# Optimization experiments

Measured on AMD Instinct MI355X. Metric: run time of the kernel, lower is better.

Reference implementation:

```python
import jax, jax.numpy as jnp
import numpy as np

DIM = 2048
SEQ = 8192
NUM_HEADS = 16
PROJ_DIM = DIM // 4  # proj_ratio = 4.0
EPS = 1e-5


def setup_inputs() -> dict:
    key = jax.random.key(0)
    ks = jax.random.split(key, 8)
    s = 0.02  # param init scale
    return {
        "x": jax.random.normal(ks[0], (SEQ, DIM), jnp.float32),
        "q": jax.random.normal(ks[1], (1, DIM), jnp.float32),
        "W_kv": jax.random.normal(ks[2], (2 * DIM, DIM), jnp.float32) * s,
        "b_kv": jax.random.normal(ks[3], (2 * DIM,), jnp.float32) * s,
        "W_p1": jax.random.normal(ks[4], (PROJ_DIM, DIM), jnp.float32) * s,
        "b_p1": jax.random.normal(ks[5], (PROJ_DIM,), jnp.float32) * s,
        "W_p2": jax.random.normal(ks[6], (DIM, PROJ_DIM), jnp.float32) * s,
        "b_p2": jax.random.normal(ks[7], (DIM,), jnp.float32) * s,
        "ln_w": jnp.ones((PROJ_DIM,), jnp.float32),
        "ln_b": jnp.zeros((PROJ_DIM,), jnp.float32),
    }


def reference(x, q, W_kv, b_kv, W_p1, b_p1, W_p2, b_p2, ln_w, ln_b):
    seq, dim = x.shape
    h = NUM_HEADS
    d = dim // h

    # kv projection: [s, 2*dim]; split '(n h d)' with n leading -> k = first dim cols
    kv = x @ W_kv.T + b_kv
    k = kv[:, :dim].reshape(seq, h, d).transpose(1, 0, 2)   # [h, s, d]
    v = kv[:, dim:].reshape(seq, h, d).transpose(1, 0, 2)   # [h, s, d]
    qh = q.reshape(h, 1, d)                                  # '1 (h d) -> h 1 d'

    # single-query attention (qk_norm=False -> Identity norms)
    attn = jnp.einsum('hqd,hkd->hqk', qh, k) / jnp.sqrt(jnp.asarray(d, x.dtype))
    attn = jax.nn.softmax(attn, axis=-1)                     # [h, 1, s]
    x1 = jnp.einsum('hqk,hkd->hqd', attn, v)                 # [h, 1, d]
    x1 = x1.transpose(1, 0, 2).reshape(1, dim)               # 'h s d -> s (h d)'

    # proj MLP: proj1 -> LayerNorm -> relu -> proj2
    h1 = x1 @ W_p1.T + b_p1                                  # [1, proj_dim]
    mu = jnp.mean(h1, axis=-1, keepdims=True)
    var = jnp.mean(jnp.square(h1 - mu), axis=-1, keepdims=True)
    h1 = (h1 - mu) / jnp.sqrt(var + EPS) * ln_w + ln_b
    x1 = jax.nn.relu(h1) @ W_p2.T + b_p2                     # [1, dim]

    # residual broadcast: [s, dim] + [1, dim]
    return x + x1
```

## Files before the change

### kernel.cpp

```cpp
#include <hip/hip_runtime.h>
#include <math.h>

#define SEQ   8192
#define DIM   2048
#define NH    16
#define DH    128
#define PD    512

static constexpr float LN_EPS = 1e-5f;
static constexpr float SCALE  = 0.08838834764831845f;

typedef __bf16 bf16x8 __attribute__((ext_vector_type(8)));
typedef float  f32x4  __attribute__((ext_vector_type(4)));

static constexpr size_t OFF_QB   = 0;
static constexpr size_t OFF_SMP  = 16;
static constexpr size_t OFF_QWB  = 528;
static constexpr size_t OFF_ELOG = 16912;
static constexpr size_t OFF_PCTX = OFF_ELOG + 131072;
static constexpr size_t OFF_CTX  = OFF_PCTX + 2097152;
static constexpr size_t OFF_X1   = OFF_CTX + 32768;
static constexpr size_t OFF_H1R  = OFF_X1 + 2048;
static constexpr size_t OFF_X1F  = OFF_H1R + 512;

__global__ __launch_bounds__(256) void k_prep(const float* __restrict__ q,
                                              const float* __restrict__ Wkv,
                                              const float* __restrict__ bkv,
                                              __bf16* __restrict__ qWb,
                                              float* __restrict__ qb,
                                              float* __restrict__ smp) {
    int t = threadIdx.x;
    int h = blockIdx.x >> 4, jc = blockIdx.x & 15;
    int col = t & 127, kh = t >> 7;
    int j = jc * 128 + col;
    const float* w  = Wkv + (size_t)(h * DH + kh * 64) * DIM + j;
    const float* qh = q + h * DH + kh * 64;
    float acc = 0.f;
#pragma unroll 16
    for (int d = 0; d < 64; ++d)
        acc += qh[d] * __builtin_nontemporal_load(w + (size_t)d * DIM);
    __shared__ float part[128];
    if (kh) part[col] = acc;
    __syncthreads();
    if (!kh) qWb[h * DIM + j] = (__bf16)(acc + part[col]);
    if (jc == 0 && t < 64) {
        float p = q[h*DH + t] * bkv[h*DH + t] + q[h*DH + 64 + t] * bkv[h*DH + 64 + t];
        for (int off = 32; off; off >>= 1) p += __shfl_down(p, off);
        if (t == 0) qb[h] = p;
    }
    if (blockIdx.x == 0) { smp[t] = 0.f; smp[t + 256] = 0.f; }
}

__global__ __launch_bounds__(256) void k_logits(const float* __restrict__ x,
                                                const __bf16* __restrict__ qWb,
                                                const float* __restrict__ qb,
                                                float* __restrict__ elogT,
                                                float* __restrict__ smp) {
    const int t = threadIdx.x;
    const int w = t >> 6, lane = t & 63;
    const int r = lane & 15, quad = lane >> 4;
    const int s0 = blockIdx.x * 16;
    __shared__ float dpart[4][64][4];
    __shared__ float hsum[NH];
    if (t < NH) hsum[t] = 0.f;

    const float*  xrow = x + (size_t)(s0 + r) * DIM + quad * 8;
    const __bf16* brow = qWb + r * DIM + quad * 8;
    const int kbase = w * 512;

    f32x4 acc = {0.f, 0.f, 0.f, 0.f};
#pragma unroll 4
    for (int i = 0; i < 16; ++i) {
        int k = kbase + i * 32;
        float4 xa = *(const float4*)(xrow + k);
        float4 xb = *(const float4*)(xrow + k + 4);
        bf16x8 af;
        af[0] = (__bf16)xa.x; af[1] = (__bf16)xa.y;
        af[2] = (__bf16)xa.z; af[3] = (__bf16)xa.w;
        af[4] = (__bf16)xb.x; af[5] = (__bf16)xb.y;
        af[6] = (__bf16)xb.z; af[7] = (__bf16)xb.w;
        bf16x8 bf = *(const bf16x8*)(brow + k);
        acc = __builtin_amdgcn_mfma_f32_16x16x32_bf16(af, bf, acc, 0, 0, 0);
    }
    dpart[w][lane][0] = acc[0];
    dpart[w][lane][1] = acc[1];
    dpart[w][lane][2] = acc[2];
    dpart[w][lane][3] = acc[3];
    __syncthreads();

    {
        const int lane2 = t & 63, reg = t >> 6;
        const int h = lane2 & 15, sl = (lane2 >> 4) * 4 + reg;
        float v = dpart[0][lane2][reg] + dpart[1][lane2][reg]
                + dpart[2][lane2][reg] + dpart[3][lane2][reg];
        float e = __expf((v + qb[h]) * SCALE);
        elogT[(size_t)(s0 + sl) * NH + h] = e;
        atomicAdd(&hsum[h], e);
    }
    __syncthreads();
    if (t < NH) atomicAdd(&smp[t * 32 + (blockIdx.x & 31)], hsum[t]);
}

__global__ __launch_bounds__(256) void k_wctx(const float* __restrict__ x,
                                              const float* __restrict__ elogT,
                                              float* __restrict__ pctx) {
    const int b = blockIdx.x, t = threadIdx.x;
    const int sc = b >> 3, jc = b & 7;
    const int s0 = sc * 128;
    const int j = jc * 256 + t;

    __shared__ float att[128 * NH];
    for (int i = t; i < 128 * NH; i += 256)
        att[i] = elogT[(size_t)s0 * NH + i];
    __syncthreads();

    float acc[NH];
#pragma unroll
    for (int h = 0; h < NH; ++h) acc[h] = 0.f;
    const float* xp = x + (size_t)s0 * DIM + j;
#pragma unroll 4
    for (int rr = 0; rr < 128; ++rr) {
        float xv = xp[(size_t)rr * DIM];
        const f32x4* ar = (const f32x4*)(att + rr * NH);
        f32x4 a0 = ar[0], a1 = ar[1], a2 = ar[2], a3 = ar[3];
        float aa[NH];
        *(f32x4*)&aa[0] = a0; *(f32x4*)&aa[4]  = a1;
        *(f32x4*)&aa[8] = a2; *(f32x4*)&aa[12] = a3;
#pragma unroll
        for (int h = 0; h < NH; ++h) acc[h] += xv * aa[h];
    }
#pragma unroll
    for (int h = 0; h < NH; ++h)
        __builtin_nontemporal_store(acc[h],
            &pctx[((size_t)(sc * NH + h)) * DIM + j]);
}

__global__ __launch_bounds__(256) void k_ctxred(const float* __restrict__ pctx,
                                                const float* __restrict__ smp,
                                                float* __restrict__ ctx) {
    const int b = blockIdx.x, t = threadIdx.x;
    const int h = b >> 5;
    const int col = t & 63, ch = t >> 6;
    __shared__ float sInv;
    __shared__ float psum[4][64];
    const size_t idx = (size_t)b * 64 + col;
    float s = 0.f;
#pragma unroll
    for (int i = 0; i < 16; ++i)
        s += __builtin_nontemporal_load(
                 &pctx[(size_t)(ch * 16 + i) * (NH * DIM) + idx]);
    psum[ch][col] = s;
    if (t < 32) {
        float v = smp[h * 32 + t];
        for (int off = 16; off; off >>= 1) v += __shfl_xor(v, off);
        if (t == 0) sInv = 1.0f / v;
    }
    __syncthreads();
    if (ch == 0)
        ctx[idx] = (psum[0][col] + psum[1][col] + psum[2][col] + psum[3][col]) * sInv;
}

__global__ __launch_bounds__(256) void k_x1(const float* __restrict__ Wkv,
                                            const float* __restrict__ bkv,
                                            const float* __restrict__ ctx,
                                            float* __restrict__ x1) {
    int row = blockIdx.x * 4 + (threadIdx.x >> 6);
    int lane = threadIdx.x & 63;
    const float* w = Wkv + (size_t)(DIM + row) * DIM;
    const float* c = ctx + (row >> 7) * DIM;
    float acc = 0.f;
#pragma unroll
    for (int k = 0; k < 8; ++k) {
        int j = k * 256 + lane * 4;
        f32x4 wv = __builtin_nontemporal_load((const f32x4*)&w[j]);
        f32x4 cv = *(const f32x4*)&c[j];
        acc += wv[0]*cv[0] + wv[1]*cv[1] + wv[2]*cv[2] + wv[3]*cv[3];
    }
    for (int off = 32; off; off >>= 1) acc += __shfl_xor(acc, off);
    if (lane == 0) x1[row] = acc + bkv[DIM + row];
}

__global__ __launch_bounds__(256) void k_h1(const float* __restrict__ Wp1,
                                            const float* __restrict__ bp1,
                                            const float* __restrict__ x1,
                                            float* __restrict__ h1raw) {
    int row = blockIdx.x * 4 + (threadIdx.x >> 6);
    int lane = threadIdx.x & 63;
    const float* w = Wp1 + (size_t)row * DIM;
    float acc = 0.f;
#pragma unroll
    for (int k = 0; k < 8; ++k) {
        int j = k * 256 + lane * 4;
        f32x4 wv = __builtin_nontemporal_load((const f32x4*)&w[j]);
        f32x4 cv = *(const f32x4*)&x1[j];
        acc += wv[0]*cv[0] + wv[1]*cv[1] + wv[2]*cv[2] + wv[3]*cv[3];
    }
    for (int off = 32; off; off >>= 1) acc += __shfl_xor(acc, off);
    if (lane == 0) h1raw[row] = acc + bp1[row];
}

__global__ __launch_bounds__(256) void k_x1f(const float* __restrict__ Wp2,
                                             const float* __restrict__ bp2,
                                             const float* __restrict__ h1raw,
                                             const float* __restrict__ lnw,
                                             const float* __restrict__ lnb,
                                             float* __restrict__ x1f) {
    int row = blockIdx.x * 4 + (threadIdx.x >> 6);
    int lane = threadIdx.x & 63;
    int j = lane * 8;
    float4 va = *(const float4*)&h1raw[j];
    float4 vb = *(const float4*)&h1raw[j + 4];
    float s = va.x + va.y + va.z + va.w + vb.x + vb.y + vb.z + vb.w;
    for (int off = 32; off; off >>= 1) s += __shfl_xor(s, off);
    float mu = s * (1.0f / PD);
    float dx[8];
    dx[0]=va.x-mu; dx[1]=va.y-mu; dx[2]=va.z-mu; dx[3]=va.w-mu;
    dx[4]=vb.x-mu; dx[5]=vb.y-mu; dx[6]=vb.z-mu; dx[7]=vb.w-mu;
    float s2 = 0.f;
#pragma unroll
    for (int i = 0; i < 8; ++i) s2 += dx[i] * dx[i];
    for (int off = 32; off; off >>= 1) s2 += __shfl_xor(s2, off);
    float rstd = rsqrtf(s2 * (1.0f / PD) + LN_EPS);
    float4 lw0 = *(const float4*)&lnw[j], lw1 = *(const float4*)&lnw[j + 4];
    float4 lb0 = *(const float4*)&lnb[j], lb1 = *(const float4*)&lnb[j + 4];
    float hln[8];
    hln[0]=fmaxf(dx[0]*rstd*lw0.x+lb0.x,0.f); hln[1]=fmaxf(dx[1]*rstd*lw0.y+lb0.y,0.f);
    hln[2]=fmaxf(dx[2]*rstd*lw0.z+lb0.z,0.f); hln[3]=fmaxf(dx[3]*rstd*lw0.w+lb0.w,0.f);
    hln[4]=fmaxf(dx[4]*rstd*lw1.x+lb1.x,0.f); hln[5]=fmaxf(dx[5]*rstd*lw1.y+lb1.y,0.f);
    hln[6]=fmaxf(dx[6]*rstd*lw1.z+lb1.z,0.f); hln[7]=fmaxf(dx[7]*rstd*lw1.w+lb1.w,0.f);
    const float* w = Wp2 + (size_t)row * PD + j;
    f32x4 w0 = __builtin_nontemporal_load((const f32x4*)w);
    f32x4 w1 = __builtin_nontemporal_load((const f32x4*)(w + 4));
    float acc = w0[0]*hln[0] + w0[1]*hln[1] + w0[2]*hln[2] + w0[3]*hln[3]
              + w1[0]*hln[4] + w1[1]*hln[5] + w1[2]*hln[6] + w1[3]*hln[7];
    for (int off = 32; off; off >>= 1) acc += __shfl_xor(acc, off);
    if (lane == 0) x1f[row] = acc + bp2[row];
}

__global__ __launch_bounds__(256) void k_out(const float* __restrict__ x,
                                             const float* __restrict__ x1f,
                                             float* __restrict__ out) {
    size_t i = (size_t)blockIdx.x * 512 + threadIdx.x;
    f32x4 xv = ((const f32x4*)x)[i];
    f32x4 a  = ((const f32x4*)x1f)[(int)(i & 511)];
    __builtin_nontemporal_store(xv + a, (f32x4*)out + i);
    size_t i2 = i + 256;
    f32x4 xv2 = ((const f32x4*)x)[i2];
    f32x4 a2  = ((const f32x4*)x1f)[(int)(i2 & 511)];
    __builtin_nontemporal_store(xv2 + a2, (f32x4*)out + i2);
}

extern "C" void kernel_launch(void* const* d_in, const int* in_sizes, int n_in,
                              void* d_out, int out_size, void* d_ws, size_t ws_size,
                              hipStream_t stream) {
    const float* x    = (const float*)d_in[0];
    const float* q    = (const float*)d_in[1];
    const float* Wkv  = (const float*)d_in[2];
    const float* bkv  = (const float*)d_in[3];
    const float* Wp1  = (const float*)d_in[4];
    const float* bp1  = (const float*)d_in[5];
    const float* Wp2  = (const float*)d_in[6];
    const float* bp2  = (const float*)d_in[7];
    const float* lnw  = (const float*)d_in[8];
    const float* lnb  = (const float*)d_in[9];
    float* out = (float*)d_out;
    float* ws  = (float*)d_ws;

    float*  qb    = ws + OFF_QB;
    float*  smp   = ws + OFF_SMP;
    __bf16* qWb   = (__bf16*)(ws + OFF_QWB);
    float*  elogT = ws + OFF_ELOG;
    float*  pctx  = ws + OFF_PCTX;
    float*  ctx   = ws + OFF_CTX;
    float*  x1    = ws + OFF_X1;
    float*  h1raw = ws + OFF_H1R;
    float*  x1f   = ws + OFF_X1F;

    k_prep  <<<256, 256, 0, stream>>>(q, Wkv, bkv, qWb, qb, smp);
    k_logits<<<512, 256, 0, stream>>>(x, qWb, qb, elogT, smp);
    k_wctx  <<<512, 256, 0, stream>>>(x, elogT, pctx);
    k_ctxred<<<512, 256, 0, stream>>>(pctx, smp, ctx);
    k_x1    <<<512, 256, 0, stream>>>(Wkv, bkv, ctx, x1);
    k_h1    <<<128, 256, 0, stream>>>(Wp1, bp1, x1, h1raw);
    k_x1f   <<<512, 256, 0, stream>>>(Wp2, bp2, h1raw, lnw, lnb, x1f);
    k_out   <<<8192, 256, 0, stream>>>(x, x1f, out);
}
```

Baseline: 214.2 us.

## Replace bf16 MFMA logits kernel with fp32 VALU register-resident qW dot products

After: 249.1 us. +16.3%, slower.

```diff
diff --git a/kernel.cpp b/kernel.cpp
--- a/kernel.cpp
+++ b/kernel.cpp
@@ -10,13 +10,12 @@
 static constexpr float LN_EPS = 1e-5f;
 static constexpr float SCALE  = 0.08838834764831845f;
 
-typedef __bf16 bf16x8 __attribute__((ext_vector_type(8)));
-typedef float  f32x4  __attribute__((ext_vector_type(4)));
+typedef float f32x4 __attribute__((ext_vector_type(4)));
 
 static constexpr size_t OFF_QB   = 0;
 static constexpr size_t OFF_SMP  = 16;
-static constexpr size_t OFF_QWB  = 528;
-static constexpr size_t OFF_ELOG = 16912;
+static constexpr size_t OFF_QWT  = 528;
+static constexpr size_t OFF_ELOG = OFF_QWT + 32768;
 static constexpr size_t OFF_PCTX = OFF_ELOG + 131072;
 static constexpr size_t OFF_CTX  = OFF_PCTX + 2097152;
 static constexpr size_t OFF_X1   = OFF_CTX + 32768;
@@ -26,7 +25,7 @@
 __global__ __launch_bounds__(256) void k_prep(const float* __restrict__ q,
                                               const float* __restrict__ Wkv,
                                               const float* __restrict__ bkv,
-                                              __bf16* __restrict__ qWb,
+                                              float* __restrict__ qWT,
                                               float* __restrict__ qb,
                                               float* __restrict__ smp) {
     int t = threadIdx.x;
@@ -42,7 +41,7 @@
     __shared__ float part[128];
     if (kh) part[col] = acc;
     __syncthreads();
-    if (!kh) qWb[h * DIM + j] = (__bf16)(acc + part[col]);
+    if (!kh) qWT[(size_t)j * NH + h] = acc + part[col];
     if (jc == 0 && t < 64) {
         float p = q[h*DH + t] * bkv[h*DH + t] + q[h*DH + 64 + t] * bkv[h*DH + 64 + t];
         for (int off = 32; off; off >>= 1) p += __shfl_down(p, off);
@@ -51,54 +50,65 @@
     if (blockIdx.x == 0) { smp[t] = 0.f; smp[t + 256] = 0.f; }
 }
 
-__global__ __launch_bounds__(256) void k_logits(const float* __restrict__ x,
-                                                const __bf16* __restrict__ qWb,
-                                                const float* __restrict__ qb,
-                                                float* __restrict__ elogT,
-                                                float* __restrict__ smp) {
-    const int t = threadIdx.x;
+__global__ __launch_bounds__(256) void k_logv(const float* __restrict__ x,
+                                              const float* __restrict__ qWT,
+                                              const float* __restrict__ qb,
+                                              float* __restrict__ elogT,
+                                              float* __restrict__ smp) {
+    const int b = blockIdx.x, t = threadIdx.x;
     const int w = t >> 6, lane = t & 63;
-    const int r = lane & 15, quad = lane >> 4;
-    const int s0 = blockIdx.x * 16;
-    __shared__ float dpart[4][64][4];
+    const int s0 = b * 8;
+
+    __shared__ float wsum[8][4][NH];
     __shared__ float hsum[NH];
     if (t < NH) hsum[t] = 0.f;
 
-    const float*  xrow = x + (size_t)(s0 + r) * DIM + quad * 8;
-    const __bf16* brow = qWb + r * DIM + quad * 8;
-    const int kbase = w * 512;
-
-    f32x4 acc = {0.f, 0.f, 0.f, 0.f};
-#pragma unroll 4
-    for (int i = 0; i < 16; ++i) {
-        int k = kbase + i * 32;
-        float4 xa = *(const float4*)(xrow + k);
-        float4 xb = *(const float4*)(xrow + k + 4);
-        bf16x8 af;
-        af[0] = (__bf16)xa.x; af[1] = (__bf16)xa.y;
-        af[2] = (__bf16)xa.z; af[3] = (__bf16)xa.w;
-        af[4] = (__bf16)xb.x; af[5] = (__bf16)xb.y;
-        af[6] = (__bf16)xb.z; af[7] = (__bf16)xb.w;
-        bf16x8 bf = *(const bf16x8*)(brow + k);
-        acc = __builtin_amdgcn_mfma_f32_16x16x32_bf16(af, bf, acc, 0, 0, 0);
-    }
-    dpart[w][lane][0] = acc[0];
-    dpart[w][lane][1] = acc[1];
-    dpart[w][lane][2] = acc[2];
-    dpart[w][lane][3] = acc[3];
-    __syncthreads();
-
-    {
-        const int lane2 = t & 63, reg = t >> 6;
-        const int h = lane2 & 15, sl = (lane2 >> 4) * 4 + reg;
-        float v = dpart[0][lane2][reg] + dpart[1][lane2][reg]
-                + dpart[2][lane2][reg] + dpart[3][lane2][reg];
+    float qw[128];
+#pragma unroll
+    for (int g = 0; g < 2; ++g)
+#pragma unroll
+        for (int dj = 0; dj < 4; ++dj) {
+            const float* p = qWT + (size_t)(g * 1024 + t * 4 + dj) * NH;
+#pragma unroll
+            for (int hq = 0; hq < 4; ++hq)
+                *(f32x4*)&qw[g * 64 + dj * 16 + hq * 4] = *(const f32x4*)(p + hq * 4);
+        }
+
+#pragma unroll 2
+    for (int r = 0; r < 8; ++r) {
+        const float* xr = x + (size_t)(s0 + r) * DIM + t * 4;
+        f32x4 xv0 = *(const f32x4*)xr;
+        f32x4 xv1 = *(const f32x4*)(xr + 1024);
+        float acc[NH];
+#pragma unroll
+        for (int h = 0; h < NH; ++h) acc[h] = 0.f;
+#pragma unroll
+        for (int dj = 0; dj < 4; ++dj)
+#pragma unroll
+            for (int h = 0; h < NH; ++h) {
+                acc[h] += xv0[dj] * qw[dj * 16 + h];
+                acc[h] += xv1[dj] * qw[64 + dj * 16 + h];
+            }
+#pragma unroll
+        for (int off = 32; off; off >>= 1)
+#pragma unroll
+            for (int h = 0; h < NH; ++h)
+                acc[h] += __shfl_xor(acc[h], off);
+        if (lane == 0) {
+#pragma unroll
+            for (int h = 0; h < NH; ++h) wsum[r][w][h] = acc[h];
+        }
+    }
+    __syncthreads();
+    if (t < 128) {
+        const int r = t >> 4, h = t & 15;
+        float v = wsum[r][0][h] + wsum[r][1][h] + wsum[r][2][h] + wsum[r][3][h];
         float e = __expf((v + qb[h]) * SCALE);
-        elogT[(size_t)(s0 + sl) * NH + h] = e;
+        elogT[(size_t)(s0 + r) * NH + h] = e;
         atomicAdd(&hsum[h], e);
     }
     __syncthreads();
-    if (t < NH) atomicAdd(&smp[t * 32 + (blockIdx.x & 31)], hsum[t]);
+    if (t < NH) atomicAdd(&smp[t * 32 + (b & 31)], hsum[t]);
 }
 
 __global__ __launch_bounds__(256) void k_wctx(const float* __restrict__ x,
@@ -266,22 +276,22 @@
     float* out = (float*)d_out;
     float* ws  = (float*)d_ws;
 
-    float*  qb    = ws + OFF_QB;
-    float*  smp   = ws + OFF_SMP;
-    __bf16* qWb   = (__bf16*)(ws + OFF_QWB);
-    float*  elogT = ws + OFF_ELOG;
-    float*  pctx  = ws + OFF_PCTX;
-    float*  ctx   = ws + OFF_CTX;
-    float*  x1    = ws + OFF_X1;
-    float*  h1raw = ws + OFF_H1R;
-    float*  x1f   = ws + OFF_X1F;
-
-    k_prep  <<<256, 256, 0, stream>>>(q, Wkv, bkv, qWb, qb, smp);
-    k_logits<<<512, 256, 0, stream>>>(x, qWb, qb, elogT, smp);
-    k_wctx  <<<512, 256, 0, stream>>>(x, elogT, pctx);
-    k_ctxred<<<512, 256, 0, stream>>>(pctx, smp, ctx);
-    k_x1    <<<512, 256, 0, stream>>>(Wkv, bkv, ctx, x1);
-    k_h1    <<<128, 256, 0, stream>>>(Wp1, bp1, x1, h1raw);
-    k_x1f   <<<512, 256, 0, stream>>>(Wp2, bp2, h1raw, lnw, lnb, x1f);
+    float* qb    = ws + OFF_QB;
+    float* smp   = ws + OFF_SMP;
+    float* qWT   = ws + OFF_QWT;
+    float* elogT = ws + OFF_ELOG;
+    float* pctx  = ws + OFF_PCTX;
+    float* ctx   = ws + OFF_CTX;
+    float* x1    = ws + OFF_X1;
+    float* h1raw = ws + OFF_H1R;
+    float* x1f   = ws + OFF_X1F;
+
+    k_prep  <<<256,  256, 0, stream>>>(q, Wkv, bkv, qWT, qb, smp);
+    k_logv  <<<1024, 256, 0, stream>>>(x, qWT, qb, elogT, smp);
+    k_wctx  <<<512,  256, 0, stream>>>(x, elogT, pctx);
+    k_ctxred<<<512,  256, 0, stream>>>(pctx, smp, ctx);
+    k_x1    <<<512,  256, 0, stream>>>(Wkv, bkv, ctx, x1);
+    k_h1    <<<128,  256, 0, stream>>>(Wp1, bp1, x1, h1raw);
+    k_x1f   <<<512,  256, 0, stream>>>(Wp2, bp2, h1raw, lnw, lnb, x1f);
     k_out   <<<8192, 256, 0, stream>>>(x, x1f, out);
 }
```
